# Kernel tuning notes

Measured on AMD Instinct MI355X. Metric: run time of the kernel, lower is better.

The kernel has to match this reference:

```python
import jax, jax.numpy as jnp
import numpy as np

B, S, D, MEM, STRIDE = 8, 8192, 128, 128, 64

def setup_inputs() -> dict:
    key = jax.random.key(0)
    ks = jax.random.split(key, 6)
    scale = 0.01  # matches nn.init.normal_(w, 0.0, 0.01)
    x = jax.random.normal(ks[0], (B, S, D), dtype=jnp.float32)
    Wq = scale * jax.random.normal(ks[1], (D, D), dtype=jnp.float32)
    Wk = scale * jax.random.normal(ks[2], (D, D), dtype=jnp.float32)
    Wv = scale * jax.random.normal(ks[3], (MEM, D), dtype=jnp.float32)
    Wg_w = jnp.zeros((1, D), dtype=jnp.float32)       # W_g weight init zeros
    Wg_b = jnp.full((1,), -2.0, dtype=jnp.float32)    # W_g bias init -2.0
    Wout = scale * jax.random.normal(ks[4], (D, MEM), dtype=jnp.float32)
    return {"x": x, "Wq": Wq, "Wk": Wk, "Wv": Wv, "Wg_w": Wg_w, "Wg_b": Wg_b, "Wout": Wout}

def reference(x, Wq, Wk, Wv, Wg_w, Wg_b, Wout):
    b, s, d = x.shape
    nC = s // STRIDE  # S assumed divisible by stride
    q = x @ Wq.T                                  # [B,S,D]
    k = x @ Wk.T                                  # [B,S,D]
    v = x @ Wv.T                                  # [B,S,MEM]
    g = jax.nn.sigmoid(x @ Wg_w.T + Wg_b)         # [B,S,1]
    # chunk: leading scan axis nC
    qc = q.reshape(b, nC, STRIDE, d).transpose(1, 0, 2, 3)
    kc = k.reshape(b, nC, STRIDE, d).transpose(1, 0, 2, 3)
    vc = v.reshape(b, nC, STRIDE, MEM).transpose(1, 0, 2, 3)
    gc = g.reshape(b, nC, STRIDE, 1).transpose(1, 0, 2, 3)

    def step(M, chunk):
        qch, kch, vch, gch = chunk
        reads = jnp.einsum('bsd,bdm->bsm', qch, M)              # read before write
        write = jnp.einsum('bsd,bsm->bdm', kch * gch, vch)      # gated outer-product
        avg_gate = gch.mean(axis=1, keepdims=True)              # [B,1,1]
        M_new = (1.0 - avg_gate) * M + write
        return M_new, reads

    M0 = jnp.zeros((b, d, MEM), dtype=x.dtype)
    _, reads = jax.lax.scan(step, M0, (qc, kc, vc, gc))         # [nC,B,STRIDE,MEM]
    out = reads.transpose(1, 0, 2, 3).reshape(b, s, MEM)
    return out @ Wout.T                                         # [B,S,D]
```

## Files before the change

### kernel.cpp

```cpp
#include <hip/hip_runtime.h>

#define Bn 8
#define Sn 8192
#define Dn 128
#define NCn 128

typedef _Float16 f16;
typedef f16 f16x2 __attribute__((ext_vector_type(2)));
typedef f16 f16x4 __attribute__((ext_vector_type(4)));
typedef float f32x4 __attribute__((ext_vector_type(4)));

static __device__ __forceinline__ f32x4 mfma16(f16x4 a, f16x4 b, f32x4 c) {
  return __builtin_amdgcn_mfma_f32_16x16x16f16(a, b, c, 0, 0, 0);
}

union UU { uint4 u; f16x2 h[4]; };


static __device__ __forceinline__ void stage_T136(const float* __restrict__ src,
                                                  f16* __restrict__ dst, int tid) {
#pragma unroll
  for (int ii = 0; ii < 4; ++ii) {
    int id = ii * 256 + tid;
    int r4 = id >> 5, c4 = id & 31;
    float4 row[4];
#pragma unroll
    for (int i = 0; i < 4; ++i)
      row[i] = *(const float4*)(src + (r4 * 4 + i) * 128 + c4 * 4);
#pragma unroll
    for (int j = 0; j < 4; ++j) {
      f16x4 col = {(f16)(((const float*)&row[0])[j]), (f16)(((const float*)&row[1])[j]),
                   (f16)(((const float*)&row[2])[j]), (f16)(((const float*)&row[3])[j])};
      *(f16x4*)&dst[(c4 * 4 + j) * 136 + r4 * 4] = col;
    }
  }
}

__global__ __launch_bounds__(256) void k_prep(
    const float* __restrict__ Wq, const float* __restrict__ Wk,
    const float* __restrict__ Wv, const float* __restrict__ Wout,
    f16* __restrict__ Amat, f16* __restrict__ r2) {
  __shared__ __align__(16) f16 Ls[32 * 136];
  __shared__ __align__(16) f16 R[128 * 136];
  const int blk = blockIdx.x;
  const int which = blk >> 2, j = blk & 3;
  const int tid = threadIdx.x;
  if (which == 0) {
    int kb = tid >> 3, cb = tid & 7;
    float4 row[4];
#pragma unroll
    for (int i = 0; i < 4; ++i)
      row[i] = *(const float4*)(Wq + (kb * 4 + i) * 128 + j * 32 + cb * 4);
#pragma unroll
    for (int jj = 0; jj < 4; ++jj) {
      f16x4 col = {(f16)(((const float*)&row[0])[jj]), (f16)(((const float*)&row[1])[jj]),
                   (f16)(((const float*)&row[2])[jj]), (f16)(((const float*)&row[3])[jj])};
      *(f16x4*)&Ls[(cb * 4 + jj) * 136 + kb * 4] = col;
    }
    stage_T136(Wk, R, tid);
  } else {
    int r = tid >> 3, sub = tid & 7;
#pragma unroll
    for (int i = 0; i < 4; ++i) {
      int col = sub * 4 + i * 32;
      float4 v = *(const float4*)(Wout + (j * 32 + r) * 128 + col);
      f16x4 h = {(f16)v.x, (f16)v.y, (f16)v.z, (f16)v.w};
      *(f16x4*)&Ls[r * 136 + col] = h;
    }
    stage_T136(Wv, R, tid);
  }
  __syncthreads();
  const int w = tid >> 6, lane = tid & 63, r16 = lane & 15, g4 = lane >> 4;
  const int rt = w & 1, cb4 = (w >> 1) * 4;
  f32x4 acc[4] = {};
#pragma unroll
  for (int kk = 0; kk < 8; ++kk) {
    f16x4 af = *(f16x4*)&Ls[(rt * 16 + r16) * 136 + kk * 16 + g4 * 4];
#pragma unroll
    for (int t = 0; t < 4; ++t) {
      f16x4 bf = *(f16x4*)&R[((cb4 + t) * 16 + r16) * 136 + kk * 16 + g4 * 4];
      acc[t] = mfma16(af, bf, acc[t]);
    }
  }
  f16* dst = which ? r2 : Amat;
#pragma unroll
  for (int t = 0; t < 4; ++t)
#pragma unroll
    for (int jj = 0; jj < 4; ++jj)
      dst[(j * 32 + rt * 16 + g4 * 4 + jj) * 128 + (cb4 + t) * 16 + r16] = (f16)acc[t][jj];
}

__global__ __launch_bounds__(512, 4) void k_phase1(
    const float* __restrict__ x, const float* __restrict__ gw, const float* __restrict__ gb,
    const f16* __restrict__ Amat, const f16* __restrict__ r2,
    f16x4* __restrict__ wtg, float* __restrict__ gavg) {
  __shared__ __align__(16) f16 Xs[64][136];
  __shared__ __align__(16) f16x4 vP[4096];
  __shared__ float gs[64];
  const int h = blockIdx.x;
  const int grp = h & 127, m = h >> 7;
  const int b = grp >> 4, seg = grp & 15;
  const int c = seg * 8 + m;
  const int tid = threadIdx.x;
  {
    int s = tid >> 3, sub = tid & 7;
    const float* xrow = x + ((size_t)b * Sn + (size_t)c * 64 + s) * Dn;
    float gpart = 0.f;
#pragma unroll
    for (int i = 0; i < 4; ++i) {
      int col = sub * 4 + i * 32;
      float4 v = *(const float4*)(xrow + col);
      float4 g = *(const float4*)(gw + col);
      gpart += v.x * g.x + v.y * g.y + v.z * g.z + v.w * g.w;
      f16x4 hh = {(f16)v.x, (f16)v.y, (f16)v.z, (f16)v.w};
      *(f16x4*)&Xs[s][col] = hh;
    }
    gpart += __shfl_xor(gpart, 1);
    gpart += __shfl_xor(gpart, 2);
    gpart += __shfl_xor(gpart, 4);
    if (sub == 0) gs[s] = 1.f / (1.f + __expf(-(gpart + gb[0])));
  }
  __syncthreads();
  if (tid == 0) {
    float sum = 0.f;
#pragma unroll
    for (int i = 0; i < 64; ++i) sum += gs[i];
    gavg[b * NCn + c] = sum * (1.f / 64.f);
  }
  const int w = tid >> 6, lane = tid & 63, r16 = lane & 15, g4 = lane >> 4;

  f32x4 uacc[4] = {}, vacc[4] = {};
#pragma unroll
  for (int kk = 0; kk < 8; ++kk) {
    f16x4 bu = *(const f16x4*)&Amat[(w * 16 + r16) * 128 + kk * 16 + g4 * 4];
    f16x4 bv = *(const f16x4*)&r2[(w * 16 + r16) * 128 + kk * 16 + g4 * 4];
#pragma unroll
    for (int mr = 0; mr < 4; ++mr) {
      f16x4 af = *(f16x4*)&Xs[mr * 16 + r16][kk * 16 + g4 * 4];
      uacc[mr] = mfma16(af, bu, uacc[mr]);
      vacc[mr] = mfma16(af, bv, vacc[mr]);
    }
  }
  f16x4 ua[4];
#pragma unroll
  for (int mr = 0; mr < 4; ++mr) {
    float g0 = gs[mr * 16 + g4 * 4 + 0], g1 = gs[mr * 16 + g4 * 4 + 1];
    float g2 = gs[mr * 16 + g4 * 4 + 2], g3 = gs[mr * 16 + g4 * 4 + 3];
    f16x4 uh = {(f16)(uacc[mr][0] * g0), (f16)(uacc[mr][1] * g1),
                (f16)(uacc[mr][2] * g2), (f16)(uacc[mr][3] * g3)};
    ua[mr] = uh;
    f16x4 vh = {(f16)vacc[mr][0], (f16)vacc[mr][1], (f16)vacc[mr][2], (f16)vacc[mr][3]};
    vP[(mr * 8 + w) * 64 + lane] = vh;
  }
  __syncthreads();

  f32x4 z[8] = {};
#pragma unroll
  for (int ks = 0; ks < 4; ++ks)
#pragma unroll
    for (int ct = 0; ct < 8; ++ct)
      z[ct] = mfma16(ua[ks], vP[(ks * 8 + ct) * 64 + lane], z[ct]);

  f16x4* wdst = wtg + (size_t)(b * NCn + c) * 4096;
#pragma unroll
  for (int ct = 0; ct < 8; ++ct) {
    f16x4 zh = {(f16)z[ct][0], (f16)z[ct][1], (f16)z[ct][2], (f16)z[ct][3]};
    wdst[(w * 8 + ct) * 64 + lane] = zh;
  }
}

__global__ __launch_bounds__(256) void k_scan(
    const uint* __restrict__ wtg, const float* __restrict__ gavg, uint* __restrict__ pbuf) {
  const int blk = blockIdx.x;
  const int b = blk >> 5;
  const int e = (blk & 31) * 256 + threadIdx.x;
  const uint* wp = wtg + (size_t)b * (NCn * 8192) + e;
  uint* pp = pbuf + (size_t)b * (15 * 8192) + e;
  const float* ga = gavg + b * NCn;
  float M0 = 0.f, M1 = 0.f;
  uint ubuf[16];
  float abuf[16];
#pragma unroll
  for (int i = 0; i < 16; ++i) {
    ubuf[i] = wp[(size_t)i * 8192];
    abuf[i] = ga[i];
  }
  for (int g = 0; g < 8; ++g) {
    uint un[16];
    float an[16];
    if (g < 7) {
#pragma unroll
      for (int i = 0; i < 16; ++i) {
        un[i] = wp[(size_t)((g + 1) * 16 + i) * 8192];
        an[i] = ga[(g + 1) * 16 + i];
      }
    }
#pragma unroll
    for (int i = 0; i < 16; ++i) {
      int cc = g * 16 + i;
      f16x2 wv = __builtin_bit_cast(f16x2, ubuf[i]);
      float dd = 1.f - abuf[i];
      M0 = dd * M0 + (float)wv[0];
      M1 = dd * M1 + (float)wv[1];
      if ((cc & 7) == 7 && cc < 120) {
        f16x2 mv = {(f16)M0, (f16)M1};
        pp[(size_t)(cc >> 3) * 8192] = __builtin_bit_cast(uint, mv);
      }
    }
    if (g < 7) {
#pragma unroll
      for (int i = 0; i < 16; ++i) { ubuf[i] = un[i]; abuf[i] = an[i]; }
    }
  }
}

__global__ __launch_bounds__(512, 4) void k_out(
    const float* __restrict__ x, const uint4* __restrict__ wtg4,
    const uint4* __restrict__ pbuf4, const float* __restrict__ gavg,
    float* __restrict__ outp) {
  __shared__ __align__(16) f16 Xs[64][136];
  __shared__ __align__(16) f16x4 zP[4096];
  const int h = blockIdx.x;
  const int grp = h & 127, m = h >> 7;
  const int b = grp >> 4, seg = grp & 15;
  const int c = seg * 8 + m;
  const int tid = threadIdx.x;
  {
    int s = tid >> 3, sub = tid & 7;
    const float* xrow = x + ((size_t)b * Sn + (size_t)c * 64 + s) * Dn;
#pragma unroll
    for (int i = 0; i < 4; ++i) {
      int col = sub * 4 + i * 32;
      float4 v = *(const float4*)(xrow + col);
      f16x4 hh = {(f16)v.x, (f16)v.y, (f16)v.z, (f16)v.w};
      *(f16x4*)&Xs[s][col] = hh;
    }
  }
  float d[8], sfac[8];
#pragma unroll
  for (int t = 0; t < 8; ++t)
    d[t] = (t < m) ? (1.f - gavg[b * NCn + seg * 8 + t]) : 1.f;
  sfac[7] = 1.f;
#pragma unroll
  for (int t = 6; t >= 0; --t) sfac[t] = sfac[t + 1] * d[t + 1];
  const float sP = sfac[0] * d[0];

  const uint4* Zp[8];
#pragma unroll
  for (int t = 0; t < 8; ++t)
    Zp[t] = wtg4 + (size_t)(b * NCn + seg * 8 + t) * 2048;
  const uint4* Pp = pbuf4 + (size_t)(b * 15 + (seg > 0 ? seg - 1 : 0)) * 2048;

#pragma unroll
  for (int i = 0; i < 4; ++i) {
    int idx = tid + i * 512;
    float a8[8] = {0.f, 0.f, 0.f, 0.f, 0.f, 0.f, 0.f, 0.f};
    if (seg > 0) {
      UU z; z.u = Pp[idx];
#pragma unroll
      for (int q = 0; q < 4; ++q) {
        a8[2 * q] += sP * (float)z.h[q][0];
        a8[2 * q + 1] += sP * (float)z.h[q][1];
      }
    }
#pragma unroll
    for (int t = 0; t < 8; ++t)
      if (t < m) {
        UU z; z.u = Zp[t][idx];
#pragma unroll
        for (int q = 0; q < 4; ++q) {
          a8[2 * q] += sfac[t] * (float)z.h[q][0];
          a8[2 * q + 1] += sfac[t] * (float)z.h[q][1];
        }
      }
    UU o;
#pragma unroll
    for (int q = 0; q < 4; ++q)
      o.h[q] = (f16x2){(f16)a8[2 * q], (f16)a8[2 * q + 1]};
    ((uint4*)zP)[idx] = o.u;
  }
  __syncthreads();
  const int w = tid >> 6, lane = tid & 63, r16 = lane & 15, g4 = lane >> 4;
  const int mr = w & 3, cb = (w >> 2) * 4;
  f32x4 acc[4] = {};
#pragma unroll
  for (int kk = 0; kk < 8; ++kk) {
    f16x4 af = *(f16x4*)&Xs[mr * 16 + r16][kk * 16 + g4 * 4];
#pragma unroll
    for (int t = 0; t < 4; ++t)
      acc[t] = mfma16(af, zP[(kk * 8 + cb + t) * 64 + lane], acc[t]);
  }
  float* obase = outp + ((size_t)b * Sn + (size_t)c * 64 + mr * 16 + g4 * 4) * Dn;
#pragma unroll
  for (int t = 0; t < 4; ++t)
#pragma unroll
    for (int j = 0; j < 4; ++j)
      obase[(size_t)j * Dn + (cb + t) * 16 + r16] = acc[t][j];
}

extern "C" void kernel_launch(void* const* d_in, const int* in_sizes, int n_in,
                              void* d_out, int out_size, void* d_ws, size_t ws_size,
                              hipStream_t stream) {
  const float* x = (const float*)d_in[0];
  const float* Wq = (const float*)d_in[1];
  const float* Wk = (const float*)d_in[2];
  const float* Wv = (const float*)d_in[3];
  const float* gw = (const float*)d_in[4];
  const float* gb = (const float*)d_in[5];
  const float* Wout = (const float*)d_in[6];

  char* ws = (char*)d_ws;
  f16* Amat = (f16*)(ws + 0);
  f16* r2 = (f16*)(ws + 32768);
  float* gavg = (float*)(ws + 65536);
  f16* wtg = (f16*)(ws + 69632);
  f16* pbuf = (f16*)(ws + 69632 + 33554432);

  k_prep<<<dim3(8), dim3(256), 0, stream>>>(Wq, Wk, Wv, Wout, Amat, r2);
  k_phase1<<<dim3(Bn * NCn), dim3(512), 0, stream>>>(x, gw, gb, Amat, r2, (f16x4*)wtg, gavg);
  k_scan<<<dim3(256), dim3(256), 0, stream>>>((const uint*)wtg, gavg, (uint*)pbuf);
  k_out<<<dim3(Bn * NCn), dim3(512), 0, stream>>>(x, (const uint4*)wtg, (const uint4*)pbuf,
                                                  gavg, (float*)d_out);
}
```

Measured before the change: 65.21 us.

## Shrink LDS staging, raise occupancy, split prep into tiles, deepen scan prefetch

k_prep is rewritten as 128 single-wave blocks, each computing one 16x16 tile directly from global memory with no LDS staging. k_phase1 and k_out halve their vP/zP LDS buffers and raise the launch-bounds wave target from 4 to 8. k_out now builds and consumes the blended memory matrix in two K-halves with an extra barrier. k_scan prefetches 32 chunks per stage instead of 16. The goal is higher occupancy and more memory-level parallelism, paid for with more register pressure and extra synchronisation. The phase1 change is only partly visible, so its coherence is uncertain.

After: 64.29 us. About the same (-1.4%).

```diff
diff --git a/kernel.cpp b/kernel.cpp
--- a/kernel.cpp
+++ b/kernel.cpp
@@ -17,85 +17,50 @@
 union UU { uint4 u; f16x2 h[4]; };
 
 
-static __device__ __forceinline__ void stage_T136(const float* __restrict__ src,
-                                                  f16* __restrict__ dst, int tid) {
-#pragma unroll
-  for (int ii = 0; ii < 4; ++ii) {
-    int id = ii * 256 + tid;
-    int r4 = id >> 5, c4 = id & 31;
-    float4 row[4];
-#pragma unroll
-    for (int i = 0; i < 4; ++i)
-      row[i] = *(const float4*)(src + (r4 * 4 + i) * 128 + c4 * 4);
-#pragma unroll
-    for (int j = 0; j < 4; ++j) {
-      f16x4 col = {(f16)(((const float*)&row[0])[j]), (f16)(((const float*)&row[1])[j]),
-                   (f16)(((const float*)&row[2])[j]), (f16)(((const float*)&row[3])[j])};
-      *(f16x4*)&dst[(c4 * 4 + j) * 136 + r4 * 4] = col;
-    }
-  }
-}
-
-__global__ __launch_bounds__(256) void k_prep(
+__global__ __launch_bounds__(64) void k_prep(
     const float* __restrict__ Wq, const float* __restrict__ Wk,
     const float* __restrict__ Wv, const float* __restrict__ Wout,
     f16* __restrict__ Amat, f16* __restrict__ r2) {
-  __shared__ __align__(16) f16 Ls[32 * 136];
-  __shared__ __align__(16) f16 R[128 * 136];
   const int blk = blockIdx.x;
-  const int which = blk >> 2, j = blk & 3;
-  const int tid = threadIdx.x;
+  const int which = blk >> 6;
+  const int t = blk & 63, ti = t >> 3, tj = t & 7;
+  const int lane = threadIdx.x & 63, r16 = lane & 15, g4 = lane >> 4;
+  f32x4 acc = {};
   if (which == 0) {
-    int kb = tid >> 3, cb = tid & 7;
-    float4 row[4];
-#pragma unroll
-    for (int i = 0; i < 4; ++i)
-      row[i] = *(const float4*)(Wq + (kb * 4 + i) * 128 + j * 32 + cb * 4);
-#pragma unroll
-    for (int jj = 0; jj < 4; ++jj) {
-      f16x4 col = {(f16)(((const float*)&row[0])[jj]), (f16)(((const float*)&row[1])[jj]),
-                   (f16)(((const float*)&row[2])[jj]), (f16)(((const float*)&row[3])[jj])};
-      *(f16x4*)&Ls[(cb * 4 + jj) * 136 + kb * 4] = col;
-    }
-    stage_T136(Wk, R, tid);
+#pragma unroll
+    for (int kk = 0; kk < 8; ++kk) {
+      f16x4 af, bf;
+#pragma unroll
+      for (int j = 0; j < 4; ++j) {
+        af[j] = (f16)Wq[(kk * 16 + g4 * 4 + j) * 128 + ti * 16 + r16];
+        bf[j] = (f16)Wk[(kk * 16 + g4 * 4 + j) * 128 + tj * 16 + r16];
+      }
+      acc = mfma16(af, bf, acc);
+    }
   } else {
-    int r = tid >> 3, sub = tid & 7;
-#pragma unroll
-    for (int i = 0; i < 4; ++i) {
-      int col = sub * 4 + i * 32;
-      float4 v = *(const float4*)(Wout + (j * 32 + r) * 128 + col);
-      f16x4 h = {(f16)v.x, (f16)v.y, (f16)v.z, (f16)v.w};
-      *(f16x4*)&Ls[r * 136 + col] = h;
-    }
-    stage_T136(Wv, R, tid);
-  }
-  __syncthreads();
-  const int w = tid >> 6, lane = tid & 63, r16 = lane & 15, g4 = lane >> 4;
-  const int rt = w & 1, cb4 = (w >> 1) * 4;
-  f32x4 acc[4] = {};
-#pragma unroll
-  for (int kk = 0; kk < 8; ++kk) {
-    f16x4 af = *(f16x4*)&Ls[(rt * 16 + r16) * 136 + kk * 16 + g4 * 4];
-#pragma unroll
-    for (int t = 0; t < 4; ++t) {
-      f16x4 bf = *(f16x4*)&R[((cb4 + t) * 16 + r16) * 136 + kk * 16 + g4 * 4];
-      acc[t] = mfma16(af, bf, acc[t]);
+#pragma unroll
+    for (int kk = 0; kk < 8; ++kk) {
+      f16x4 af, bf;
+      float4 a4 = *(const float4*)(Wout + (ti * 16 + r16) * 128 + kk * 16 + g4 * 4);
+      af[0] = (f16)a4.x; af[1] = (f16)a4.y; af[2] = (f16)a4.z; af[3] = (f16)a4.w;
+#pragma unroll
+      for (int j = 0; j < 4; ++j)
+        bf[j] = (f16)Wv[(kk * 16 + g4 * 4 + j) * 128 + tj * 16 + r16];
+      acc = mfma16(af, bf, acc);
     }
   }
   f16* dst = which ? r2 : Amat;
 #pragma unroll
-  for (int t = 0; t < 4; ++t)
-#pragma unroll
-    for (int jj = 0; jj < 4; ++jj)
-      dst[(j * 32 + rt * 16 + g4 * 4 + jj) * 128 + (cb4 + t) * 16 + r16] = (f16)acc[t][jj];
-}
-
-__global__ __launch_bounds__(512, 4) void k_phase1(
+  for (int j = 0; j < 4; ++j)
+    dst[(ti * 16 + g4 * 4 + j) * 128 + tj * 16 + r16] = (f16)acc[j];
+}
+
+__global__ __launch_bounds__(512, 8) void k_phase1(
     const float* __restrict__ x, const float* __restrict__ gw, const float* __restrict__ gb,
     const f16* __restrict__ Amat, const f16* __restrict__ r2,
     f16x4* __restrict__ wtg, float* __restrict__ gavg) {
   __shared__ __align__(16) f16 Xs[64][136];
-  __shared__ __align__(16) f16x4 vP[4096];
+  __shared__ __align__(16) f16x4 vP[2048];
   __shared__ float gs[64];
   const int h = blockIdx.x;
   const int grp = h & 127, m = h >> 7;
@@ -178,26 +143,26 @@
   uint* pp = pbuf + (size_t)b * (15 * 8192) + e;
   const float* ga = gavg + b * NCn;
   float M0 = 0.f, M1 = 0.f;
-  uint ubuf[16];
-  float abuf[16];
-#pragma unroll
-  for (int i = 0; i < 16; ++i) {
+  uint ubuf[32];
+  float abuf[32];
+#pragma unroll
+  for (int i = 0; i < 32; ++i) {
     ubuf[i] = wp[(size_t)i * 8192];
     abuf[i] = ga[i];
   }
-  for (int g = 0; g < 8; ++g) {
-    uint un[16];
-    float an[16];
-    if (g < 7) {
-#pragma unroll
-      for (int i = 0; i < 16; ++i) {
-        un[i] = wp[(size_t)((g + 1) * 16 + i) * 8192];
-        an[i] = ga[(g + 1) * 16 + i];
-      }
-    }
-#pragma unroll
-    for (int i = 0; i < 16; ++i) {
-      int cc = g * 16 + i;
+  for (int g = 0; g < 4; ++g) {
+    uint un[32];
+    float an[32];
+    if (g < 3) {
+#pragma unroll
+      for (int i = 0; i < 32; ++i) {
+        un[i] = wp[(size_t)((g + 1) * 32 + i) * 8192];
+        an[i] = ga[(g + 1) * 32 + i];
+      }
+    }
+#pragma unroll
+    for (int i = 0; i < 32; ++i) {
+      int cc = g * 32 + i;
       f16x2 wv = __builtin_bit_cast(f16x2, ubuf[i]);
       float dd = 1.f - abuf[i];
       M0 = dd * M0 + (float)wv[0];
@@ -207,19 +172,19 @@
         pp[(size_t)(cc >> 3) * 8192] = __builtin_bit_cast(uint, mv);
       }
     }
-    if (g < 7) {
-#pragma unroll
-      for (int i = 0; i < 16; ++i) { ubuf[i] = un[i]; abuf[i] = an[i]; }
-    }
-  }
-}
-
-__global__ __launch_bounds__(512, 4) void k_out(
+    if (g < 3) {
+#pragma unroll
+      for (int i = 0; i < 32; ++i) { ubuf[i] = un[i]; abuf[i] = an[i]; }
+    }
+  }
+}
+
+__global__ __launch_bounds__(512, 8) void k_out(
     const float* __restrict__ x, const uint4* __restrict__ wtg4,
     const uint4* __restrict__ pbuf4, const float* __restrict__ gavg,
     float* __restrict__ outp) {
   __shared__ __align__(16) f16 Xs[64][136];
-  __shared__ __align__(16) f16x4 zP[4096];
+  __shared__ __align__(16) f16x4 zP[2048];
   const int h = blockIdx.x;
   const int grp = h & 127, m = h >> 7;
   const int b = grp >> 4, seg = grp & 15;
@@ -245,50 +210,53 @@
   for (int t = 6; t >= 0; --t) sfac[t] = sfac[t + 1] * d[t + 1];
   const float sP = sfac[0] * d[0];
 
-  const uint4* Zp[8];
-#pragma unroll
-  for (int t = 0; t < 8; ++t)
-    Zp[t] = wtg4 + (size_t)(b * NCn + seg * 8 + t) * 2048;
+  const uint4* Zbase = wtg4 + (size_t)(b * NCn + seg * 8) * 2048;
   const uint4* Pp = pbuf4 + (size_t)(b * 15 + (seg > 0 ? seg - 1 : 0)) * 2048;
 
-#pragma unroll
-  for (int i = 0; i < 4; ++i) {
-    int idx = tid + i * 512;
-    float a8[8] = {0.f, 0.f, 0.f, 0.f, 0.f, 0.f, 0.f, 0.f};
-    if (seg > 0) {
-      UU z; z.u = Pp[idx];
-#pragma unroll
-      for (int q = 0; q < 4; ++q) {
-        a8[2 * q] += sP * (float)z.h[q][0];
-        a8[2 * q + 1] += sP * (float)z.h[q][1];
-      }
-    }
-#pragma unroll
-    for (int t = 0; t < 8; ++t)
-      if (t < m) {
-        UU z; z.u = Zp[t][idx];
-#pragma unroll
-        for (int q = 0; q < 4; ++q) {
-          a8[2 * q] += sfac[t] * (float)z.h[q][0];
-          a8[2 * q + 1] += sfac[t] * (float)z.h[q][1];
-        }
-      }
-    UU o;
-#pragma unroll
-    for (int q = 0; q < 4; ++q)
-      o.h[q] = (f16x2){(f16)a8[2 * q], (f16)a8[2 * q + 1]};
-    ((uint4*)zP)[idx] = o.u;
-  }
-  __syncthreads();
   const int w = tid >> 6, lane = tid & 63, r16 = lane & 15, g4 = lane >> 4;
   const int mr = w & 3, cb = (w >> 2) * 4;
   f32x4 acc[4] = {};
-#pragma unroll
-  for (int kk = 0; kk < 8; ++kk) {
-    f16x4 af = *(f16x4*)&Xs[mr * 16 + r16][kk * 16 + g4 * 4];
-#pragma unroll
-    for (int t = 0; t < 4; ++t)
-      acc[t] = mfma16(af, zP[(kk * 8 + cb + t) * 64 + lane], acc[t]);
+
+#pragma unroll
+  for (int half = 0; half < 2; ++half) {
+    if (half) __syncthreads();
+#pragma unroll
+    for (int i = 0; i < 2; ++i) {
+      int idx = tid + i * 512;
+      int src = half * 1024 + idx;
+      float a8[8] = {0.f, 0.f, 0.f, 0.f, 0.f, 0.f, 0.f, 0.f};
+      if (seg > 0) {
+        UU z; z.u = Pp[src];
+#pragma unroll
+        for (int q = 0; q < 4; ++q) {
+          a8[2 * q] += sP * (float)z.h[q][0];
+          a8[2 * q + 1] += sP * (float)z.h[q][1];
+        }
+      }
+#pragma unroll
+      for (int t = 0; t < 8; ++t)
+        if (t < m) {
+          UU z; z.u = Zbase[(size_t)t * 2048 + src];
+#pragma unroll
+          for (int q = 0; q < 4; ++q) {
+            a8[2 * q] += sfac[t] * (float)z.h[q][0];
+            a8[2 * q + 1] += sfac[t] * (float)z.h[q][1];
+          }
+        }
+      UU o;
+#pragma unroll
+      for (int q = 0; q < 4; ++q)
+        o.h[q] = (f16x2){(f16)a8[2 * q], (f16)a8[2 * q + 1]};
+      ((uint4*)zP)[idx] = o.u;
+    }
+    __syncthreads();
+#pragma unroll
+    for (int kk = 0; kk < 4; ++kk) {
+      f16x4 af = *(f16x4*)&Xs[mr * 16 + r16][(half * 4 + kk) * 16 + g4 * 4];
+#pragma unroll
+      for (int t = 0; t < 4; ++t)
+        acc[t] = mfma16(af, zP[(kk * 8 + cb + t) * 64 + lane], acc[t]);
+    }
   }
   float* obase = outp + ((size_t)b * Sn + (size_t)c * 64 + mr * 16 + g4 * 4) * Dn;
 #pragma unroll
@@ -316,7 +284,7 @@
   f16* wtg = (f16*)(ws + 69632);
   f16* pbuf = (f16*)(ws + 69632 + 33554432);
 
-  k_prep<<<dim3(8), dim3(256), 0, stream>>>(Wq, Wk, Wv, Wout, Amat, r2);
+  k_prep<<<dim3(128), dim3(64), 0, stream>>>(Wq, Wk, Wv, Wout, Amat, r2);
   k_phase1<<<dim3(Bn * NCn), dim3(512), 0, stream>>>(x, gw, gb, Amat, r2, (f16x4*)wtg, gavg);
   k_scan<<<dim3(256), dim3(256), 0, stream>>>((const uint*)wtg, gavg, (uint*)pbuf);
   k_out<<<dim3(Bn * NCn), dim3(512), 0, stream>>>(x, (const uint4*)wtg, (const uint4*)pbuf,
```
